# Optimization experiments

Measured on AMD Instinct MI355X. Metric: run time of the kernel, lower is better.

The kernel has to match this reference:

```python
import jax, jax.numpy as jnp
import numpy as np

B, T, D, R, DFF = 4, 4096, 1024, 128, 4096
WINDOW = 1024
EPS = 1e-6


def rmsnorm(x, w):
    x32 = x.astype(jnp.float32)
    rms = jax.lax.rsqrt(jnp.mean(x32 * x32, axis=-1, keepdims=True) + EPS)
    return (x32 * rms).astype(x.dtype) * w


def rope(x, cos, sin):
    # x: (B, T, R); cos/sin: (T, R//2)
    d = x.shape[-1] // 2
    x1, x2 = x[..., :d], x[..., d:]
    return jnp.concatenate([x1 * cos + x2 * sin, -x1 * sin + x2 * cos], axis=-1)


def setup_inputs() -> dict:
    key = jax.random.key(0)
    ks = jax.random.split(key, 12)
    s = 0.02  # realistic weight scale
    return {
        "x": jax.random.normal(ks[0], (B, T, D), jnp.float32),
        "Uq": jax.random.normal(ks[1], (R, D), jnp.float32) * s,
        "Uk": jax.random.normal(ks[2], (R, D), jnp.float32) * s,
        "Uv": jax.random.normal(ks[3], (R, D), jnp.float32) * s,
        "cos": jnp.cos(jnp.outer(jnp.arange(T, dtype=jnp.float32),
                                 1.0 / (10000.0 ** (jnp.arange(R // 2, dtype=jnp.float32) / (R // 2))))),
        "sin": jnp.sin(jnp.outer(jnp.arange(T, dtype=jnp.float32),
                                 1.0 / (10000.0 ** (jnp.arange(R // 2, dtype=jnp.float32) / (R // 2))))),
        "ln1_w": jnp.ones((D,), jnp.float32),
        "ln2_w": jnp.ones((D,), jnp.float32),
        "Wo": jax.random.normal(ks[4], (D, R), jnp.float32) * s,
        "w1": jax.random.normal(ks[5], (DFF, D), jnp.float32) * s,
        "w3": jax.random.normal(ks[6], (DFF, D), jnp.float32) * s,
        "w2": jax.random.normal(ks[7], (D, DFF), jnp.float32) * s,
        "window_size": WINDOW,
    }


def reference(x, Uq, Uk, Uv, cos, sin, ln1_w, ln2_w, Wo, w1, w3, w2, window_size):
    Bx, Tx, _ = x.shape
    rank = Uq.shape[0]
    normed = rmsnorm(x, ln1_w)
    q = rope(normed @ Uq.T, cos, sin)  # (B, T, R)
    k = rope(normed @ Uk.T, cos, sin)
    v = normed @ Uv.T
    # windowed causal single-head SDPA
    scale = 1.0 / jnp.sqrt(jnp.float32(rank))
    scores = jnp.einsum("btr,bsr->bts", q, k) * scale  # (B, T, T)
    row = jnp.arange(Tx)[:, None]
    col = jnp.arange(Tx)[None, :]
    mask = (col <= row) & ((row - col) <= window_size)
    scores = jnp.where(mask, scores, jnp.float32(-jnp.inf))
    attn = jax.nn.softmax(scores, axis=-1)
    y = jnp.einsum("bts,bsr->btr", attn, v)  # (B, T, R)
    x = x + y @ Wo.T
    h = rmsnorm(x, ln2_w)
    ffn = ((h @ w1.T) * jax.nn.silu(h @ w3.T)) @ w2.T
    return x + ffn
```

## Files before the change

kernel.cpp:

```cpp
#include <hip/hip_runtime.h>
#include <hip/hip_bf16.h>
#include <stdint.h>

#define BT   16384
#define TT   4096
#define NB   4
#define DD   1024
#define RR   128
#define DFFC 4096

typedef __bf16 bf16_8 __attribute__((ext_vector_type(8)));
typedef float  f32x4  __attribute__((ext_vector_type(4)));

__device__ __forceinline__ void async16(const void* g, void* l) {
  __builtin_amdgcn_global_load_lds((__attribute__((address_space(1))) void*)(g),
                                   (__attribute__((address_space(3))) void*)(l),
                                   16, 0, 0);
}

__global__ __launch_bounds__(256) void cvt_k(const float* __restrict__ src,
                                             __hip_bfloat16* __restrict__ dst, int n4) {
  const int i = blockIdx.x * 256 + threadIdx.x;
  if (i >= n4) return;
  const float4 v = ((const float4*)src)[i];
  __hip_bfloat16* o = dst + (size_t)i * 4;
  o[0] = __float2bfloat16(v.x);
  o[1] = __float2bfloat16(v.y);
  o[2] = __float2bfloat16(v.z);
  o[3] = __float2bfloat16(v.w);
}

__global__ __launch_bounds__(256) void rmsnorm_k(const float* __restrict__ x,
                                                 const float* __restrict__ wgt,
                                                 __hip_bfloat16* __restrict__ out) {
  const int row = blockIdx.x;
  const int t = threadIdx.x;
  const float4 v = ((const float4*)(x + (size_t)row * DD))[t];
  float ss = v.x*v.x + v.y*v.y + v.z*v.z + v.w*v.w;
  #pragma unroll
  for (int m = 1; m < 64; m <<= 1) ss += __shfl_xor(ss, m, 64);
  __shared__ float red[4];
  if ((t & 63) == 0) red[t >> 6] = ss;
  __syncthreads();
  ss = red[0] + red[1] + red[2] + red[3];
  const float rms = rsqrtf(ss * (1.0f / DD) + 1e-6f);
  const float4 wv = ((const float4*)wgt)[t];
  __hip_bfloat16* o = out + (size_t)row * DD + t * 4;
  o[0] = __float2bfloat16(v.x * rms * wv.x);
  o[1] = __float2bfloat16(v.y * rms * wv.y);
  o[2] = __float2bfloat16(v.z * rms * wv.z);
  o[3] = __float2bfloat16(v.w * rms * wv.w);
}

__global__ __launch_bounds__(256) void rope_k(const __hip_bfloat16* __restrict__ qkv,
                                              const float* __restrict__ cosb,
                                              const float* __restrict__ sinb,
                                              __hip_bfloat16* __restrict__ qr,
                                              __hip_bfloat16* __restrict__ kr) {
  const int idx = blockIdx.x * 256 + threadIdx.x;
  const int row = idx >> 6;
  const int i = idx & 63;
  const int tpos = row & (TT - 1);
  const float c = cosb[tpos * 64 + i];
  const float s = sinb[tpos * 64 + i];
  const size_t base = (size_t)row * 384;
  const float q1 = __bfloat162float(qkv[base + i]);
  const float q2 = __bfloat162float(qkv[base + 64 + i]);
  const float k1 = __bfloat162float(qkv[base + 128 + i]);
  const float k2 = __bfloat162float(qkv[base + 192 + i]);
  const size_t ob = (size_t)row * 128;
  qr[ob + i]      = __float2bfloat16( q1 * c + q2 * s);
  qr[ob + 64 + i] = __float2bfloat16(-q1 * s + q2 * c);
  kr[ob + i]      = __float2bfloat16( k1 * c + k2 * s);
  kr[ob + 64 + i] = __float2bfloat16(-k1 * s + k2 * c);
}

__global__ __launch_bounds__(256) void vtrans_k(const __hip_bfloat16* __restrict__ qkv,
                                                __hip_bfloat16* __restrict__ Vt) {
  const int b = blockIdx.y, t0 = blockIdx.x * 64, t = threadIdx.x;
  #pragma unroll
  for (int i = 0; i < 4; ++i) {
    const int flat8 = i * 256 + t;
    const int row = flat8 >> 4;
    const int d8 = (flat8 & 15) * 8;
    const bf16_8 v = *(const bf16_8*)&qkv[((size_t)(b * TT + t0 + row)) * 384 + 256 + d8];
    #pragma unroll
    for (int j = 0; j < 8; ++j)
      ((__bf16*)Vt)[((size_t)(b * 128 + d8 + j)) * TT + t0 + row] = v[j];
  }
}

enum { EPI_BF16 = 0, EPI_RESID = 1, EPI_GATE = 2 };

template <int EPI>
__global__ __launch_bounds__(256) void gemm_bt(
    const __hip_bfloat16* __restrict__ A,
    const __hip_bfloat16* __restrict__ Bw,
    const float* __restrict__ resid,
    const __hip_bfloat16* __restrict__ gate,
    __hip_bfloat16* __restrict__ outb,
    float* __restrict__ outf,
    int N, int K) {
  __shared__ __hip_bfloat16 As[128 * 64];
  __shared__ __hip_bfloat16 Bs[128 * 64];
  const int t = threadIdx.x;
  const int w = t >> 6, lane = t & 63;
  const int wm = w >> 1, wn = w & 1;
  const int quad = lane >> 4, l16 = lane & 15;
  const int m0 = blockIdx.y * 128, n0 = blockIdx.x * 128;

  const __hip_bfloat16* Ab = A + (size_t)m0 * K;
  const __hip_bfloat16* Bb = Bw + (size_t)n0 * K;

  const int rloc = w * 8 + (lane >> 3);
  const int c0 = (((lane & 7) ^ ((lane >> 3) & 7)) << 3);
  const int swz = (l16 & 7);

  f32x4 acc[4][4] = {};

  for (int k0 = 0; k0 < K; k0 += 64) {
    #pragma unroll
    for (int j = 0; j < 4; ++j) {
      async16(Ab + (size_t)(j * 32 + rloc) * K + k0 + c0, &As[j * 2048 + w * 512]);
      async16(Bb + (size_t)(j * 32 + rloc) * K + k0 + c0, &Bs[j * 2048 + w * 512]);
    }
    __syncthreads();
    #pragma unroll
    for (int kc = 0; kc < 2; ++kc) {
      bf16_8 af[4], bfr[4];
      #pragma unroll
      for (int i = 0; i < 4; ++i) {
        const int pos = (((kc * 4 + quad) ^ swz) << 3);
        af[i]  = *(const bf16_8*)&As[(wm * 64 + i * 16 + l16) * 64 + pos];
        bfr[i] = *(const bf16_8*)&Bs[(wn * 64 + i * 16 + l16) * 64 + pos];
      }
      #pragma unroll
      for (int mt = 0; mt < 4; ++mt) {
        #pragma unroll
        for (int nt = 0; nt < 4; ++nt)
          acc[mt][nt] = __builtin_amdgcn_mfma_f32_16x16x32_bf16(af[mt], bfr[nt], acc[mt][nt], 0, 0, 0);
      }
    }
    __syncthreads();
  }

  #pragma unroll
  for (int mt = 0; mt < 4; ++mt) {
    #pragma unroll
    for (int nt = 0; nt < 4; ++nt) {
      #pragma unroll
      for (int r = 0; r < 4; ++r) {
        const int row = m0 + wm * 64 + mt * 16 + quad * 4 + r;
        const int col = n0 + wn * 64 + nt * 16 + l16;
        const size_t idx = (size_t)row * N + col;
        const float v = acc[mt][nt][r];
        if (EPI == EPI_BF16) {
          outb[idx] = __float2bfloat16(v);
        } else if (EPI == EPI_RESID) {
          outf[idx] = resid[idx] + v;
        } else {
          const float sv = v / (1.0f + __expf(-v));
          outb[idx] = __float2bfloat16(__bfloat162float(gate[idx]) * sv);
        }
      }
    }
  }
}

#define G256_BAR()  asm volatile("s_barrier" ::: "memory")
#define G256_VMW4() asm volatile("s_waitcnt vmcnt(4)" ::: "memory")
#define G256_VMW0() asm volatile("s_waitcnt vmcnt(0)" ::: "memory")

#define G256_DSA(mh_) \
  { _Pragma("unroll") for (int mt = 0; mt < 4; ++mt) { \
      const int rb_ = (rbA + (mh_) * 64 + mt * 16) * 64; \
      a[mt][0] = *(const bf16_8*)&Ac[rb_ + p0]; \
      a[mt][1] = *(const bf16_8*)&Ac[rb_ + p1]; } }

#define G256_DSB(nh_) \
  { _Pragma("unroll") for (int nt = 0; nt < 2; ++nt) { \
      const int rb_ = (rbB + (nh_) * 32 + nt * 16) * 64; \
      b[nt][0] = *(const bf16_8*)&Bc[rb_ + p0]; \
      b[nt][1] = *(const bf16_8*)&Bc[rb_ + p1]; } }

#define G256_MMA(mh_, nh_) \
  { __builtin_amdgcn_s_setprio(1); \
    _Pragma("unroll") for (int kk = 0; kk < 2; ++kk) \
      _Pragma("unroll") for (int mt = 0; mt < 4; ++mt) \
        _Pragma("unroll") for (int nt = 0; nt < 2; ++nt) \
          acc[(mh_) * 4 + mt][(nh_) * 2 + nt] = __builtin_amdgcn_mfma_f32_16x16x32_bf16( \
              a[mt][kk], b[nt][kk], acc[(mh_) * 4 + mt][(nh_) * 2 + nt], 0, 0, 0); \
    __builtin_amdgcn_s_setprio(0); }

#define G256_TILE(CUR, kt_) { \
    const __hip_bfloat16* Ac = As[CUR]; \
    const __hip_bfloat16* Bc = Bs[CUR]; \
    const int nb_ = (CUR) ^ 1; \
    const bool pf = ((kt_) + 1) < NT; \
    const int kn = ((kt_) + 1) << 6; \
    if (!pf) { G256_VMW0(); G256_BAR(); } \
    G256_DSA(0); G256_DSB(0); if (pf) { stageA(0, nb_, kn); } \
    G256_BAR(); G256_MMA(0, 0); G256_VMW4(); G256_BAR(); \
    G256_DSB(1); if (pf) { stageB(0, nb_, kn); } \
    G256_BAR(); G256_MMA(0, 1); G256_VMW4(); G256_BAR(); \
    G256_DSA(1); if (pf) { stageB(1, nb_, kn); } \
    G256_BAR(); G256_MMA(1, 1); G256_VMW4(); G256_BAR(); \
    G256_DSB(0); if (pf) { stageA(1, nb_, kn); } \
    G256_BAR(); G256_MMA(1, 0); G256_VMW4(); G256_BAR(); \
  }

template <int EPI>
__global__ __launch_bounds__(512, 2) void gemm256(
    const __hip_bfloat16* __restrict__ A,
    const __hip_bfloat16* __restrict__ Bw,
    const float* __restrict__ resid,
    const __hip_bfloat16* __restrict__ gate,
    __hip_bfloat16* __restrict__ outb,
    float* __restrict__ outf,
    int N, int K) {
  __shared__ __hip_bfloat16 As[2][256 * 64];
  __shared__ __hip_bfloat16 Bs[2][256 * 64];
  const int t = threadIdx.x;
  const int w = t >> 6, lane = t & 63;
  const int wm = w >> 2, wn = w & 3;
  const int quad = lane >> 4, l16 = lane & 15;

  const int gx = gridDim.x;
  const int nwg = gx * gridDim.y;
  int lin = blockIdx.y * gx + blockIdx.x;
  lin = (lin & 7) * (nwg >> 3) + (lin >> 3);
  const int m0 = (lin / gx) * 256;
  const int n0 = (lin % gx) * 256;

  const __hip_bfloat16* Ab = A + (size_t)m0 * K;
  const __hip_bfloat16* Bb = Bw + (size_t)n0 * K;

  const int rl = lane >> 3;
  const int c0 = (((lane & 7) ^ rl) << 3);

  auto stageA = [&](int h, int buf, int k0) {
    const int r0 = h * 64 + (w << 3);
    async16(Ab + (size_t)(r0 + rl) * K + k0 + c0, &As[buf][r0 * 64]);
    const int r1 = r0 + 128;
    async16(Ab + (size_t)(r1 + rl) * K + k0 + c0, &As[buf][r1 * 64]);
  };
  auto stageB = [&](int h, int buf, int k0) {
    const int s0 = (w >> 2) * 64 + h * 32 + (w & 3) * 8;
    async16(Bb + (size_t)(s0 + rl) * K + k0 + c0, &Bs[buf][s0 * 64]);
    const int s1 = s0 + 128;
    async16(Bb + (size_t)(s1 + rl) * K + k0 + c0, &Bs[buf][s1 * 64]);
  };

  const int rbA = wm * 128 + l16;
  const int rbB = wn * 64 + l16;
  const int p0 = ((quad ^ (l16 & 7)) << 3);
  const int p1 = (((4 + quad) ^ (l16 & 7)) << 3);

  f32x4 acc[8][4] = {};
  bf16_8 a[4][2], b[2][2];
  const int NT = K >> 6;

  stageA(0, 0, 0); stageB(0, 0, 0); stageB(1, 0, 0); stageA(1, 0, 0);
  G256_VMW4(); G256_BAR();

  for (int kt = 0; kt < NT; kt += 2) {
    G256_TILE(0, kt);
    G256_TILE(1, kt + 1);
  }

  #pragma unroll
  for (int mf = 0; mf < 8; ++mf) {
    #pragma unroll
    for (int nf = 0; nf < 4; ++nf) {
      #pragma unroll
      for (int r = 0; r < 4; ++r) {
        const int row = m0 + wm * 128 + mf * 16 + quad * 4 + r;
        const int col = n0 + wn * 64 + nf * 16 + l16;
        const size_t idx = (size_t)row * N + col;
        const float v = acc[mf][nf][r];
        if (EPI == EPI_BF16) {
          outb[idx] = __float2bfloat16(v);
        } else if (EPI == EPI_RESID) {
          outf[idx] = resid[idx] + v;
        } else {
          const float sv = v / (1.0f + __expf(-v));
          outb[idx] = __float2bfloat16(__bfloat162float(gate[idx]) * sv);
        }
      }
    }
  }
}

__global__ __launch_bounds__(256) void attn_k(const __hip_bfloat16* __restrict__ qr,
                                              const __hip_bfloat16* __restrict__ kr,
                                              const __hip_bfloat16* __restrict__ Vt,
                                              __hip_bfloat16* __restrict__ y,
                                              const int* __restrict__ winp) {
  __shared__ __hip_bfloat16 Ksm[64 * 128];
  __shared__ __hip_bfloat16 Vsm[128 * 64];
  __shared__ __hip_bfloat16 Psm[4 * 16 * 72];
  const int t = threadIdx.x, w = t >> 6, lane = t & 63;
  const int quad = lane >> 4, l16 = lane & 15;
  const int b = blockIdx.y, t0 = blockIdx.x * 64;
  const int tw0 = t0 + w * 16;
  const int win = *winp;
  int kb_lo = t0 - win;
  if (kb_lo < 0) kb_lo = 0;
  kb_lo &= ~63;

  bf16_8 qf[4];
  const __hip_bfloat16* qb = qr + ((size_t)(b * TT + tw0 + l16)) * 128 + quad * 8;
  #pragma unroll
  for (int kk = 0; kk < 4; ++kk) qf[kk] = *(const bf16_8*)(qb + kk * 32);

  f32x4 o[8] = {};
  float mrow[4] = {-1e30f, -1e30f, -1e30f, -1e30f};
  float lrow[4] = {0.f, 0.f, 0.f, 0.f};
  const float scale = 0.08838834764831845f;

  const int krow_loc = (w * 4) + (lane >> 4);
  const int kc = ((lane & 15) ^ (krow_loc & 15)) << 3;
  const int vloc = lane >> 3;
  const int vc = ((lane & 7) ^ vloc) << 3;

  for (int kb0 = kb_lo; kb0 <= t0; kb0 += 64) {
    const __hip_bfloat16* kbp = kr + ((size_t)(b * TT + kb0)) * 128;
    #pragma unroll
    for (int i = 0; i < 4; ++i) {
      const int krow = i * 16 + krow_loc;
      async16(kbp + (size_t)krow * 128 + kc, &Ksm[i * 2048 + w * 512]);
    }
    #pragma unroll
    for (int i = 0; i < 4; ++i) {
      const int d0 = (i * 4 + w) * 8;
      const int dr = d0 + vloc;
      async16(Vt + ((size_t)(b * 128 + dr)) * TT + kb0 + vc, &Vsm[d0 * 64]);
    }
    __syncthreads();

    f32x4 s[4] = {};
    #pragma unroll
    for (int kk = 0; kk < 4; ++kk) {
      #pragma unroll
      for (int nt = 0; nt < 4; ++nt) {
        const int cc = ((kk * 4 + quad) ^ l16) << 3;
        const bf16_8 bfrag = *(const bf16_8*)&Ksm[(nt * 16 + l16) * 128 + cc];
        s[nt] = __builtin_amdgcn_mfma_f32_16x16x32_bf16(qf[kk], bfrag, s[nt], 0, 0, 0);
      }
    }

    float mb[4] = {-1e30f, -1e30f, -1e30f, -1e30f};
    #pragma unroll
    for (int nt = 0; nt < 4; ++nt) {
      #pragma unroll
      for (int r = 0; r < 4; ++r) {
        const int tq = tw0 + quad * 4 + r;
        const int scol = kb0 + nt * 16 + l16;
        float v = s[nt][r] * scale;
        const bool ok = (scol <= tq) && (tq - scol <= win);
        v = ok ? v : -1e30f;
        s[nt][r] = v;
        mb[r] = fmaxf(mb[r], v);
      }
    }

    #pragma unroll
    for (int r = 0; r < 4; ++r) {
      float m = mb[r];
      m = fmaxf(m, __shfl_xor(m, 1, 16));
      m = fmaxf(m, __shfl_xor(m, 2, 16));
      m = fmaxf(m, __shfl_xor(m, 4, 16));
      m = fmaxf(m, __shfl_xor(m, 8, 16));
      const float mn = fmaxf(mrow[r], m);
      const float alpha = __expf(mrow[r] - mn);
      mrow[r] = mn;
      float rs = 0.f;
      #pragma unroll
      for (int nt = 0; nt < 4; ++nt) {
        const float pv = __expf(s[nt][r] - mn);
        s[nt][r] = pv;
        rs += pv;
      }
      rs += __shfl_xor(rs, 1, 16);
      rs += __shfl_xor(rs, 2, 16);
      rs += __shfl_xor(rs, 4, 16);
      rs += __shfl_xor(rs, 8, 16);
      lrow[r] = lrow[r] * alpha + rs;
      #pragma unroll
      for (int n2 = 0; n2 < 8; ++n2) o[n2][r] *= alpha;
    }

    __hip_bfloat16* pw = &Psm[w * 1152];
    #pragma unroll
    for (int nt = 0; nt < 4; ++nt) {
      #pragma unroll
      for (int r = 0; r < 4; ++r)
        pw[(quad * 4 + r) * 72 + nt * 16 + l16] = __float2bfloat16(s[nt][r]);
    }
    asm volatile("s_waitcnt lgkmcnt(0)" ::: "memory");

    #pragma unroll
    for (int kk2 = 0; kk2 < 2; ++kk2) {
      const bf16_8 pa = *(const bf16_8*)&Psm[w * 1152 + l16 * 72 + kk2 * 32 + quad * 8];
      #pragma unroll
      for (int n2 = 0; n2 < 8; ++n2) {
        const int cc = ((kk2 * 4 + quad) ^ (l16 & 7)) << 3;
        const bf16_8 vb = *(const bf16_8*)&Vsm[(n2 * 16 + l16) * 64 + cc];
        o[n2] = __builtin_amdgcn_mfma_f32_16x16x32_bf16(pa, vb, o[n2], 0, 0, 0);
      }
    }
    __syncthreads();
  }

  #pragma unroll
  for (int n2 = 0; n2 < 8; ++n2) {
    #pragma unroll
    for (int r = 0; r < 4; ++r) {
      const int row = b * TT + tw0 + quad * 4 + r;
      const int col = n2 * 16 + l16;
      y[(size_t)row * 128 + col] = __float2bfloat16(o[n2][r] / lrow[r]);
    }
  }
}

extern "C" void kernel_launch(void* const* d_in, const int* in_sizes, int n_in,
                              void* d_out, int out_size, void* d_ws, size_t ws_size,
                              hipStream_t stream) {
  const float* x    = (const float*)d_in[0];
  const float* Uq   = (const float*)d_in[1];
  const float* Uk   = (const float*)d_in[2];
  const float* Uv   = (const float*)d_in[3];
  const float* cosb = (const float*)d_in[4];
  const float* sinb = (const float*)d_in[5];
  const float* ln1  = (const float*)d_in[6];
  const float* ln2  = (const float*)d_in[7];
  const float* Wo   = (const float*)d_in[8];
  const float* w1   = (const float*)d_in[9];
  const float* w3   = (const float*)d_in[10];
  const float* w2   = (const float*)d_in[11];
  const int*   winp = (const int*)d_in[12];
  float* out = (float*)d_out;

  uint8_t* p = (uint8_t*)d_ws;
  auto take = [&](size_t bytes) {
    uint8_t* q = p;
    p += (bytes + 255) & ~(size_t)255;
    return q;
  };

  __hip_bfloat16* h1     = (__hip_bfloat16*)take((size_t)BT * DFFC * 2);
  __hip_bfloat16* gb     = h1;
  __hip_bfloat16* normed = (__hip_bfloat16*)take((size_t)BT * DD * 2);
  __hip_bfloat16* hb     = normed;
  __hip_bfloat16* qkv    = (__hip_bfloat16*)take((size_t)BT * 384 * 2);
  __hip_bfloat16* yb     = qkv;
  __hip_bfloat16* qr_    = (__hip_bfloat16*)take((size_t)BT * RR * 2);
  __hip_bfloat16* kr_    = (__hip_bfloat16*)take((size_t)BT * RR * 2);
  __hip_bfloat16* Vt     = (__hip_bfloat16*)take((size_t)BT * RR * 2);
  __hip_bfloat16* Ucat   = (__hip_bfloat16*)take((size_t)384 * DD * 2);
  __hip_bfloat16* Wob    = (__hip_bfloat16*)take((size_t)DD * RR * 2);
  __hip_bfloat16* W1b    = (__hip_bfloat16*)take((size_t)DFFC * DD * 2);
  __hip_bfloat16* W3b    = (__hip_bfloat16*)take((size_t)DFFC * DD * 2);
  __hip_bfloat16* W2b    = (__hip_bfloat16*)take((size_t)DD * DFFC * 2);
  float* x_mid = out;

  cvt_k<<<128, 256, 0, stream>>>(Uq, Ucat, RR * DD / 4);
  cvt_k<<<128, 256, 0, stream>>>(Uk, Ucat + (size_t)RR * DD, RR * DD / 4);
  cvt_k<<<128, 256, 0, stream>>>(Uv, Ucat + (size_t)2 * RR * DD, RR * DD / 4);
  cvt_k<<<128, 256, 0, stream>>>(Wo, Wob, DD * RR / 4);
  cvt_k<<<4096, 256, 0, stream>>>(w1, W1b, DFFC * DD / 4);
  cvt_k<<<4096, 256, 0, stream>>>(w3, W3b, DFFC * DD / 4);
  cvt_k<<<4096, 256, 0, stream>>>(w2, W2b, DD * DFFC / 4);

  rmsnorm_k<<<BT, 256, 0, stream>>>(x, ln1, normed);

  gemm_bt<EPI_BF16><<<dim3(3, 128), 256, 0, stream>>>(normed, Ucat, nullptr, nullptr,
                                                      qkv, nullptr, 384, DD);

  rope_k<<<BT * 64 / 256, 256, 0, stream>>>(qkv, cosb, sinb, qr_, kr_);
  vtrans_k<<<dim3(TT / 64, NB), 256, 0, stream>>>(qkv, Vt);

  attn_k<<<dim3(TT / 64, NB), 256, 0, stream>>>(qr_, kr_, Vt, yb, winp);

  gemm_bt<EPI_RESID><<<dim3(8, 128), 256, 0, stream>>>(yb, Wob, x, nullptr,
                                                       nullptr, x_mid, DD, RR);

  rmsnorm_k<<<BT, 256, 0, stream>>>(x_mid, ln2, hb);

  gemm256<EPI_BF16><<<dim3(16, 64), 512, 0, stream>>>(hb, W1b, nullptr, nullptr,
                                                      h1, nullptr, DFFC, DD);
  gemm256<EPI_GATE><<<dim3(16, 64), 512, 0, stream>>>(hb, W3b, nullptr, h1,
                                                      gb, nullptr, DFFC, DD);
  gemm256<EPI_RESID><<<dim3(4, 64), 512, 0, stream>>>(gb, W2b, x_mid, nullptr,
                                                      nullptr, out, DD, DFFC);
}
```

Before: 754.2 us.

## Fuse FFN w1 and w3 GEMMs into one dual-B kernel with SiLU-gate epilogue

Replaces the two separate 256x256 GEMMs (h@w1 written to bf16, then h@w3 with a gate epilogue that reads it back) with a single kernel. That kernel loads each A tile once and multiplies it against both W1 and W3 tiles, keeping two accumulator sets, then applies silu(g)*h1 in registers before storing. This removes one full pass over the activations and the write and re-read of the BT x DFF intermediate. In exchange the output tile shrinks to 256x128 with double the accumulators, which adds register pressure at the requested two workgroups per CU, and the kernel uses hand-placed vmcnt waits and barriers.

```diff
diff --git a/kernel.cpp b/kernel.cpp
--- a/kernel.cpp
+++ b/kernel.cpp
@@ -291,6 +291,136 @@
   }
 }
 
+#define F13_DSA() \
+  { _Pragma("unroll") for (int mt = 0; mt < 4; ++mt) { \
+      const int rb_ = (rbA + mt * 16) * 64; \
+      a[mt][0] = *(const bf16_8*)&Ac[rb_ + p0]; \
+      a[mt][1] = *(const bf16_8*)&Ac[rb_ + p1]; } }
+
+#define F13_DSB(nh_, SRC) \
+  { _Pragma("unroll") for (int nt = 0; nt < 2; ++nt) { \
+      const int rb_ = (rbB + (nh_) * 32 + nt * 16) * 64; \
+      b[nt][0] = *(const bf16_8*)&SRC[rb_ + p0]; \
+      b[nt][1] = *(const bf16_8*)&SRC[rb_ + p1]; } }
+
+#define F13_MMA(ACC, nh_) \
+  { __builtin_amdgcn_s_setprio(1); \
+    _Pragma("unroll") for (int kk = 0; kk < 2; ++kk) \
+      _Pragma("unroll") for (int mt = 0; mt < 4; ++mt) \
+        _Pragma("unroll") for (int nt = 0; nt < 2; ++nt) \
+          ACC[mt][(nh_) * 2 + nt] = __builtin_amdgcn_mfma_f32_16x16x32_bf16( \
+              a[mt][kk], b[nt][kk], ACC[mt][(nh_) * 2 + nt], 0, 0, 0); \
+    __builtin_amdgcn_s_setprio(0); }
+
+#define F13_VMW(N) asm volatile("s_waitcnt vmcnt(" #N ")" ::: "memory")
+
+#define F13_TILE(CUR, kt_) { \
+    const __hip_bfloat16* Ac  = As[CUR]; \
+    const __hip_bfloat16* B1c = B1s[CUR]; \
+    const __hip_bfloat16* B3c = B3s[CUR]; \
+    const int nb_ = (CUR) ^ 1; \
+    const bool pf = ((kt_) + 1) < NT; \
+    const int kn = ((kt_) + 1) << 6; \
+     \
+    F13_DSA(); F13_DSB(0, B1c); \
+    if (pf) { stageA2(0, nb_, kn); stageB1(nb_, kn); } \
+    G256_BAR(); F13_MMA(acc1, 0); G256_BAR(); \
+     \
+    F13_DSB(1, B1c); \
+    if (pf) { stageA2(1, nb_, kn); } \
+    G256_BAR(); F13_MMA(acc1, 1); \
+    if (pf) { F13_VMW(6); } else { F13_VMW(0); } \
+    G256_BAR(); \
+     \
+    F13_DSB(0, B3c); \
+    if (pf) { stageB3(nb_, kn); } \
+    G256_BAR(); F13_MMA(acc3, 0); G256_BAR(); \
+     \
+    F13_DSB(1, B3c); \
+    G256_BAR(); F13_MMA(acc3, 1); \
+    if (pf) { F13_VMW(2); } \
+    G256_BAR(); \
+  }
+
+__global__ __launch_bounds__(512, 2) void gemm_ffn13(
+    const __hip_bfloat16* __restrict__ A,
+    const __hip_bfloat16* __restrict__ B1w,
+    const __hip_bfloat16* __restrict__ B3w,
+    __hip_bfloat16* __restrict__ outb,
+    int N, int K) {
+  __shared__ __hip_bfloat16 As[2][256 * 64];
+  __shared__ __hip_bfloat16 B1s[2][128 * 64];
+  __shared__ __hip_bfloat16 B3s[2][128 * 64];
+  const int t = threadIdx.x;
+  const int w = t >> 6, lane = t & 63;
+  const int wm = w >> 1, wn = w & 1;
+  const int quad = lane >> 4, l16 = lane & 15;
+
+  const int gx = gridDim.x;
+  const int nwg = gx * gridDim.y;
+  int lin = blockIdx.y * gx + blockIdx.x;
+  lin = (lin & 7) * (nwg >> 3) + (lin >> 3);
+  const int m0 = (lin / gx) * 256;
+  const int n0 = (lin % gx) * 128;
+
+  const __hip_bfloat16* Ab  = A   + (size_t)m0 * K;
+  const __hip_bfloat16* B1b = B1w + (size_t)n0 * K;
+  const __hip_bfloat16* B3b = B3w + (size_t)n0 * K;
+
+  const int rl = lane >> 3;
+  const int c0 = (((lane & 7) ^ rl) << 3);
+
+  auto stageA2 = [&](int h, int buf, int k0) {
+    const int r0 = h * 128 + (w << 3);
+    async16(Ab + (size_t)(r0 + rl) * K + k0 + c0, &As[buf][r0 * 64]);
+    const int r1 = r0 + 64;
+    async16(Ab + (size_t)(r1 + rl) * K + k0 + c0, &As[buf][r1 * 64]);
+  };
+  auto stageB1 = [&](int buf, int k0) {
+    const int s0 = (w << 3);
+    async16(B1b + (size_t)(s0 + rl) * K + k0 + c0, &B1s[buf][s0 * 64]);
+    async16(B1b + (size_t)(s0 + 64 + rl) * K + k0 + c0, &B1s[buf][(s0 + 64) * 64]);
+  };
+  auto stageB3 = [&](int buf, int k0) {
+    const int s0 = (w << 3);
+    async16(B3b + (size_t)(s0 + rl) * K + k0 + c0, &B3s[buf][s0 * 64]);
+    async16(B3b + (size_t)(s0 + 64 + rl) * K + k0 + c0, &B3s[buf][(s0 + 64) * 64]);
+  };
+
+  const int rbA = wm * 64 + l16;
+  const int rbB = wn * 64 + l16;
+  const int p0 = ((quad ^ (l16 & 7)) << 3);
+  const int p1 = (((4 + quad) ^ (l16 & 7)) << 3);
+
+  f32x4 acc1[4][4] = {};
+  f32x4 acc3[4][4] = {};
+  bf16_8 a[4][2], b[2][2];
+  const int NT = K >> 6;
+
+  stageA2(0, 0, 0); stageB1(0, 0); stageA2(1, 0, 0); stageB3(0, 0);
+  F13_VMW(2); G256_BAR();
+
+  for (int kt = 0; kt < NT; kt += 2) {
+    F13_TILE(0, kt);
+    F13_TILE(1, kt + 1);
+  }
+
+  #pragma unroll
+  for (int mt = 0; mt < 4; ++mt) {
+    #pragma unroll
+    for (int nt = 0; nt < 4; ++nt) {
+      #pragma unroll
+      for (int r = 0; r < 4; ++r) {
+        const int row = m0 + wm * 64 + mt * 16 + quad * 4 + r;
+        const int col = n0 + wn * 64 + nt * 16 + l16;
+        const float g = acc3[mt][nt][r];
+        const float sv = g / (1.0f + __expf(-g));
+        outb[(size_t)row * N + col] = __float2bfloat16(acc1[mt][nt][r] * sv);
+      }
+    }
+  }
+}
+
 __global__ __launch_bounds__(256) void attn_k(const __hip_bfloat16* __restrict__ qr,
                                               const __hip_bfloat16* __restrict__ kr,
                                               const __hip_bfloat16* __restrict__ Vt,
@@ -448,8 +578,7 @@
     return q;
   };
 
-  __hip_bfloat16* h1     = (__hip_bfloat16*)take((size_t)BT * DFFC * 2);
-  __hip_bfloat16* gb     = h1;
+  __hip_bfloat16* gb     = (__hip_bfloat16*)take((size_t)BT * DFFC * 2);
   __hip_bfloat16* normed = (__hip_bfloat16*)take((size_t)BT * DD * 2);
   __hip_bfloat16* hb     = normed;
   __hip_bfloat16* qkv    = (__hip_bfloat16*)take((size_t)BT * 384 * 2);
@@ -487,10 +616,9 @@
 
   rmsnorm_k<<<BT, 256, 0, stream>>>(x_mid, ln2, hb);
 
-  gemm256<EPI_BF16><<<dim3(16, 64), 512, 0, stream>>>(hb, W1b, nullptr, nullptr,
-                                                      h1, nullptr, DFFC, DD);
-  gemm256<EPI_GATE><<<dim3(16, 64), 512, 0, stream>>>(hb, W3b, nullptr, h1,
-                                                      gb, nullptr, DFFC, DD);
+  gemm_ffn13<<<dim3(DFFC / 128, BT / 256), 512, 0, stream>>>(hb, W1b, W3b, gb,
+                                                             DFFC, DD);
+
   gemm256<EPI_RESID><<<dim3(4, 64), 512, 0, stream>>>(gb, W2b, x_mid, nullptr,
                                                       nullptr, out, DD, DFFC);
 }
```

Measured after the change: 736.8 us. 1.02x faster.
